# Kernel tuning notes

Measured on AMD Instinct MI355X. Metric: run time of the kernel, lower is better.

The kernel has to match this reference:

```python
import jax, jax.numpy as jnp
import numpy as np

N, T, DS, DA = 256, 64, 32, 8
D, H, FF = 512, 8, 2048
HD = D // H          # head_dim = 64
IN = DS + DA         # input_dim = 40
EULER_STEPS = 4


def setup_inputs():
    key = jax.random.key(0)
    ks = jax.random.split(key, 12)
    g = lambda k, shape: (jax.random.normal(k, shape) * 0.02).astype(jnp.float32)
    z = lambda *s: jnp.zeros(s, jnp.float32)
    o = lambda *s: jnp.ones(s, jnp.float32)
    return {
        "states": jax.random.normal(ks[0], (N, T, DS), jnp.float32),
        "actions": jax.random.normal(ks[1], (N, T, DA), jnp.float32),
        "time_steps": jnp.cumsum(jax.random.uniform(ks[2], (N, T + 1), jnp.float32, 0.01, 0.1), axis=1),
        "W_ode": g(ks[3], (D, D)), "b_ode": z(D),
        "W_in": g(ks[4], (IN, D)), "b_in": z(D),
        "ln_in_g": o(D), "ln_in_b": z(D),
        "W_q": g(ks[5], (D, D)), "b_q": z(D),
        "W_kv": g(ks[6], (IN + D, 2 * D + H)), "b_kv": z(2 * D + H),
        "W_out": g(ks[7], (D, D)), "b_out": z(D),
        "ln_ff_g": o(D), "ln_ff_b": z(D),
        "W_ff1": g(ks[8], (D, FF)), "b_ff1": z(FF),
        "W_ff2": g(ks[9], (FF, D)), "b_ff2": z(D),
        "W_dec": g(ks[10], (D, DS)), "b_dec": z(DS),
    }


def _ln(x, g, b):
    m = jnp.mean(x, -1, keepdims=True)
    v = jnp.mean((x - m) ** 2, -1, keepdims=True)
    return (x - m) * jax.lax.rsqrt(v + 1e-5) * g + b


def _forward(states, actions, time_steps, W_ode, b_ode, W_in, b_in, ln_in_g, ln_in_b,
             W_q, b_q, W_kv, b_kv, W_out, b_out, ln_ff_g, ln_ff_b,
             W_ff1, b_ff1, W_ff2, b_ff2, W_dec, b_dec):
    n = states.shape[0]
    # teacher forcing path (train=True, eps_decay=0): data_i = cat(states_i, actions_i)
    data_seq = jnp.concatenate([states, actions], -1).transpose(1, 0, 2)  # [T, N, IN]
    dts = (time_steps[:, 1:] - time_steps[:, :-1]).T                      # [T, N]

    def step(carry, xs):
        h1, W2 = carry            # h1: [N, D], W2: [N, H, HD, HD] fast weights
        data, dt = xs
        # integrate latent ODE over per-sample dt (fixed-step Euler, autonomous tanh MLP)
        step_dt = (dt / EULER_STEPS)[:, None]
        for _ in range(EULER_STEPS):
            h1 = h1 + step_dt * jnp.tanh(h1 @ W_ode + b_ode)
        # Hebbian fast-weight update: W2 += lr * v (x) k  (per head)
        x = jnp.concatenate([data, h1], -1)
        kvb = x @ W_kv + b_kv
        k = jax.nn.softmax(kvb[:, :D].reshape(n, H, HD), -1)
        v = jnp.tanh(kvb[:, D:2 * D]).reshape(n, H, HD)
        lr = jax.nn.sigmoid(kvb[:, 2 * D:])                    # [N, H]
        W2 = W2 + lr[:, :, None, None] * jnp.einsum('nhv,nhk->nhvk', v, k)
        # query_fast_weight
        q = _ln(data @ W_in + b_in, ln_in_g, ln_in_b) @ W_q + b_q
        q = jax.nn.softmax(q.reshape(n, H, HD), -1)
        out = jnp.einsum('nhvk,nhk->nhv', W2, q).reshape(n, D)
        out = out @ W_out + b_out
        y = _ln(out, ln_ff_g, ln_ff_b)
        out = jnp.maximum(y @ W_ff1 + b_ff1, 0.0) @ W_ff2 + b_ff2 + out  # FF block + residual
        pred = out @ W_dec + b_dec                              # decoder
        return (out, W2), pred

    h0 = jnp.zeros((n, D), states.dtype)
    W20 = jnp.zeros((n, H, HD, HD), states.dtype)
    _, preds = jax.lax.scan(step, (h0, W20), (data_seq, dts))
    return preds.transpose(1, 0, 2)  # [N, T, DS] predicted next states


def reference(states, actions, time_steps, W_ode, b_ode, W_in, b_in, ln_in_g, ln_in_b,
              W_q, b_q, W_kv, b_kv, W_out, b_out, ln_ff_g, ln_ff_b,
              W_ff1, b_ff1, W_ff2, b_ff2, W_dec, b_dec):
    return _forward(states, actions, time_steps, W_ode, b_ode, W_in, b_in, ln_in_g, ln_in_b,
                    W_q, b_q, W_kv, b_kv, W_out, b_out, ln_ff_g, ln_ff_b,
                    W_ff1, b_ff1, W_ff2, b_ff2, W_dec, b_dec)
```

## Files before the change

### kernel.cpp

```cpp
#include <hip/hip_runtime.h>

#define NS   256
#define TS   64
#define DS   32
#define DA   8
#define DD   512
#define HH   8
#define HD   64
#define FF   2048
#define INP  40
#define INPP 20
#define INPG 24
#define DP   256
#define KVKP 276
#define KVKPP 280
#define KVO  1032
#define FFP  1024

#define OFF_ODE 0
#define SZ_ODE  (32*512*8)
#define OFF_KV  (OFF_ODE+SZ_ODE)
#define SZ_KV   (35*1032*8)
#define OFF_IN  (OFF_KV+SZ_KV)
#define SZ_IN   (3*512*8)
#define OFF_Q   (OFF_IN+SZ_IN)
#define SZ_Q    (32*512*8)
#define OFF_OUT (OFF_Q+SZ_Q)
#define SZ_OUT  (32*512*8)
#define OFF_F1  (OFF_OUT+SZ_OUT)
#define SZ_F1   (32*2048*8)
#define OFF_F2  (OFF_F1+SZ_F1)
#define SZ_F2   (128*512*8)
#define OFF_DEC (OFF_F2+SZ_F2)
#define SZ_DEC  (32*32*8)

#define DEV __device__ __forceinline__

typedef _Float16 half2_t __attribute__((ext_vector_type(2)));

DEV half2_t as_h2(unsigned int u) { return __builtin_bit_cast(half2_t, u); }

DEV float dot2f(unsigned int w, unsigned int x, float acc) {
#if __has_builtin(__builtin_amdgcn_fdot2)
  return __builtin_amdgcn_fdot2(as_h2(w), as_h2(x), acc, false);
#else
  half2_t a = as_h2(w), b = as_h2(x);
  return acc + (float)a[0] * (float)b[0] + (float)a[1] * (float)b[1];
#endif
}

DEV unsigned int pack2f(float a, float b) {
  unsigned short ua = __builtin_bit_cast(unsigned short, (_Float16)a);
  unsigned short ub = __builtin_bit_cast(unsigned short, (_Float16)b);
  return ((unsigned int)ub << 16) | (unsigned int)ua;
}

DEV float fast_tanh(float x) {
  float ax = fabsf(x);
  float e  = __expf(-2.0f * ax);
  float r  = (1.0f - e) / (1.0f + e);
  return copysignf(r, x);
}

DEV float fast_sigmoid(float x) { return 1.0f / (1.0f + __expf(-x)); }

DEV float wave_max(float v) {
  #pragma unroll
  for (int o = 32; o; o >>= 1) v = fmaxf(v, __shfl_xor(v, o));
  return v;
}
DEV float wave_sum(float v) {
  #pragma unroll
  for (int o = 32; o; o >>= 1) v += __shfl_xor(v, o);
  return v;
}

DEV float dotG(const unsigned int* __restrict__ Wc, int strideG,
               const unsigned int* __restrict__ xq, int NG, float init) {
  float a0 = init, a1 = 0.f, a2 = 0.f, a3 = 0.f;
  #pragma unroll 4
  for (int g = 0; g < NG; ++g) {
    uint4 w0 = *reinterpret_cast<const uint4*>(Wc + g * strideG);
    uint4 w1 = *reinterpret_cast<const uint4*>(Wc + g * strideG + 4);
    uint4 x0 = *reinterpret_cast<const uint4*>(xq + g * 8);
    uint4 x1 = *reinterpret_cast<const uint4*>(xq + g * 8 + 4);
    a0 = dot2f(w0.x, x0.x, a0);
    a1 = dot2f(w0.y, x0.y, a1);
    a2 = dot2f(w0.z, x0.z, a2);
    a3 = dot2f(w0.w, x0.w, a3);
    a0 = dot2f(w1.x, x1.x, a0);
    a1 = dot2f(w1.y, x1.y, a1);
    a2 = dot2f(w1.z, x1.z, a2);
    a3 = dot2f(w1.w, x1.w, a3);
  }
  return (a0 + a1) + (a2 + a3);
}

__global__ void pack_wg_kernel(const float* __restrict__ src, unsigned int* __restrict__ dst,
                               int K, int KPpad, int Dout) {
  int idx = blockIdx.x * blockDim.x + threadIdx.x;
  int total = KPpad * Dout;
  if (idx >= total) return;
  int kp = idx / Dout;
  int j  = idx - kp * Dout;
  int r0 = 2 * kp, r1 = r0 + 1;
  float lo = (r0 < K) ? src[r0 * Dout + j] : 0.f;
  float hi = (r1 < K) ? src[r1 * Dout + j] : 0.f;
  int kg = kp >> 3, sub = kp & 7;
  dst[((kg * Dout + j) << 3) + sub] = pack2f(lo, hi);
}

__global__ __launch_bounds__(512) void fwp_main(
    const float* __restrict__ states, const float* __restrict__ actions,
    const float* __restrict__ tsteps,
    const float* __restrict__ b_ode, const float* __restrict__ b_in,
    const float* __restrict__ ln_in_g, const float* __restrict__ ln_in_b,
    const float* __restrict__ b_q, const float* __restrict__ b_kv,
    const float* __restrict__ b_out,
    const float* __restrict__ ln_ff_g, const float* __restrict__ ln_ff_b,
    const float* __restrict__ b_ff1, const float* __restrict__ b_ff2,
    const float* __restrict__ b_dec,
    const unsigned int* __restrict__ Wode, const unsigned int* __restrict__ Wkv,
    const unsigned int* __restrict__ Win,  const unsigned int* __restrict__ Wq,
    const unsigned int* __restrict__ Wout, const unsigned int* __restrict__ Wff1,
    const unsigned int* __restrict__ Wff2, const unsigned int* __restrict__ Wdec,
    unsigned int* __restrict__ ctrs, float* __restrict__ outp) {

  const int n = blockIdx.x, tid = threadIdx.x;
  const int w = tid >> 6, lane = tid & 63;

  __shared__ alignas(16) float        sh_h[DD];
  __shared__ alignas(16) unsigned int sh_hp[DP];
  __shared__ alignas(16) unsigned int sh_xp[KVKPP];
  __shared__ alignas(16) unsigned int sh_dp[INPG];
  __shared__ alignas(16) float        sh_t[DD];
  __shared__ alignas(16) unsigned int sh_p[DP];
  __shared__ alignas(16) float        sh_kvb[KVO];
  __shared__ alignas(16) float        sh_k[DD];
  __shared__ alignas(16) float        sh_v[DD];
  __shared__ alignas(16) float        sh_q[DD];
  __shared__ float                    sh_lr[HH];
  __shared__ alignas(16) float        sh_ff[FF];
  __shared__ alignas(16) unsigned int sh_ffp[FFP];
  __shared__ float                    sh_red[16];
  __shared__ alignas(16) float        sh_decp[512];
  __shared__ int                      sh_flag;

  float W2r[64];
  #pragma unroll
  for (int i = 0; i < 64; ++i) W2r[i] = 0.f;

  sh_h[tid] = 0.f;
  if (tid < DP) sh_hp[tid] = 0u;
  if (tid >= DP && tid < DP + (KVKPP - KVKP)) sh_xp[KVKP + (tid - DP)] = 0u;
  if (tid >= 300 && tid < 300 + (INPG - INPP)) sh_dp[INPP + (tid - 300)] = 0u;

  bool pace = true;
  unsigned int* ctr = ctrs + 16 * (n & 7);

  for (int t = 0; t < TS; ++t) {
    __syncthreads();

    if (pace) {
      if (tid == 0) {
        sh_flag = 0;
        __hip_atomic_fetch_add(ctr, 1u, __ATOMIC_RELAXED, __HIP_MEMORY_SCOPE_AGENT);
        unsigned int tgt = 32u * (unsigned int)(t + 1);
        int it = 0;
        while (__hip_atomic_load(ctr, __ATOMIC_RELAXED, __HIP_MEMORY_SCOPE_AGENT) < tgt) {
          if (++it > 4096) { sh_flag = 1; break; }
          __builtin_amdgcn_s_sleep(8);
        }
      }
      __syncthreads();
      if (sh_flag) pace = false;
    }

    if (tid < INPP) {
      int i0 = 2 * tid, i1 = i0 + 1;
      float a = (i0 < DS) ? states[(n * TS + t) * DS + i0] : actions[(n * TS + t) * DA + (i0 - DS)];
      float b = (i1 < DS) ? states[(n * TS + t) * DS + i1] : actions[(n * TS + t) * DA + (i1 - DS)];
      unsigned int p = pack2f(a, b);
      sh_xp[tid] = p;
      sh_dp[tid] = p;
    }
    const float sdt = 0.25f * (tsteps[n * (TS + 1) + t + 1] - tsteps[n * (TS + 1) + t]);

    for (int e = 0; e < 4; ++e) {
      float acc = dotG(Wode + tid * 8, DD * 8, sh_hp, 32, b_ode[tid]);
      sh_h[tid] += sdt * fast_tanh(acc);
      __syncthreads();
      if (tid < DP) sh_hp[tid] = pack2f(sh_h[2 * tid], sh_h[2 * tid + 1]);
      __syncthreads();
    }

    if (tid < DP) sh_xp[INPP + tid] = sh_hp[tid];
    __syncthreads();

    for (int j = tid; j < KVO; j += 512)
      sh_kvb[j] = dotG(Wkv + j * 8, KVO * 8, sh_xp, 35, b_kv[j]);
    __syncthreads();

    {
      float kx = sh_kvb[tid];
      float km = wave_max(kx);
      float ke = __expf(kx - km);
      float ks = wave_sum(ke);
      sh_k[tid] = ke / ks;
      sh_v[tid] = fast_tanh(sh_kvb[DD + tid]);
      if (tid < HH) sh_lr[tid] = fast_sigmoid(sh_kvb[2 * DD + tid]);
    }

    float y1 = dotG(Win + tid * 8, DD * 8, sh_dp, 3, b_in[tid]);
    {
      float s1 = y1, s2 = y1 * y1;
      #pragma unroll
      for (int o = 32; o; o >>= 1) { s1 += __shfl_xor(s1, o); s2 += __shfl_xor(s2, o); }
      if (lane == 0) { sh_red[2 * w] = s1; sh_red[2 * w + 1] = s2; }
      __syncthreads();
      s1 = 0.f; s2 = 0.f;
      #pragma unroll
      for (int i = 0; i < 8; ++i) { s1 += sh_red[2 * i]; s2 += sh_red[2 * i + 1]; }
      float m  = s1 * (1.0f / DD);
      float va = fmaxf(s2 * (1.0f / DD) - m * m, 0.f);
      float rs = rsqrtf(va + 1e-5f);
      sh_t[tid] = (y1 - m) * rs * ln_in_g[tid] + ln_in_b[tid];
    }
    __syncthreads();
    if (tid < DP) sh_p[tid] = pack2f(sh_t[2 * tid], sh_t[2 * tid + 1]);
    __syncthreads();
    {
      float qraw = dotG(Wq + tid * 8, DD * 8, sh_p, 32, b_q[tid]);
      float qm = wave_max(qraw);
      float qe = __expf(qraw - qm);
      float qs = wave_sum(qe);
      sh_q[tid] = qe / qs;
    }
    __syncthreads();

    {
      float vi  = sh_v[tid];
      float lrw = sh_lr[w];
      float lv  = lrw * vi;
      float acc = 0.f;
      const float* kb = sh_k + w * HD;
      const float* qb = sh_q + w * HD;
      #pragma unroll
      for (int jc = 0; jc < 16; ++jc) {
        float4 k4 = *reinterpret_cast<const float4*>(kb + 4 * jc);
        float4 q4 = *reinterpret_cast<const float4*>(qb + 4 * jc);
        W2r[4 * jc + 0] += lv * k4.x; acc += W2r[4 * jc + 0] * q4.x;
        W2r[4 * jc + 1] += lv * k4.y; acc += W2r[4 * jc + 1] * q4.y;
        W2r[4 * jc + 2] += lv * k4.z; acc += W2r[4 * jc + 2] * q4.z;
        W2r[4 * jc + 3] += lv * k4.w; acc += W2r[4 * jc + 3] * q4.w;
      }
      sh_t[tid] = acc;
    }
    __syncthreads();
    if (tid < DP) sh_p[tid] = pack2f(sh_t[2 * tid], sh_t[2 * tid + 1]);
    __syncthreads();

    float o1 = dotG(Wout + tid * 8, DD * 8, sh_p, 32, b_out[tid]);

    {
      float s1 = o1, s2 = o1 * o1;
      #pragma unroll
      for (int o = 32; o; o >>= 1) { s1 += __shfl_xor(s1, o); s2 += __shfl_xor(s2, o); }
      if (lane == 0) { sh_red[2 * w] = s1; sh_red[2 * w + 1] = s2; }
      __syncthreads();
      s1 = 0.f; s2 = 0.f;
      #pragma unroll
      for (int i = 0; i < 8; ++i) { s1 += sh_red[2 * i]; s2 += sh_red[2 * i + 1]; }
      float m  = s1 * (1.0f / DD);
      float va = fmaxf(s2 * (1.0f / DD) - m * m, 0.f);
      float rs = rsqrtf(va + 1e-5f);
      sh_t[tid] = (o1 - m) * rs * ln_ff_g[tid] + ln_ff_b[tid];
    }
    __syncthreads();
    if (tid < DP) sh_p[tid] = pack2f(sh_t[2 * tid], sh_t[2 * tid + 1]);
    __syncthreads();

    {
      float f0 = b_ff1[tid], f1 = b_ff1[tid + 512], f2 = b_ff1[tid + 1024], f3 = b_ff1[tid + 1536];
      #pragma unroll 2
      for (int g = 0; g < 32; ++g) {
        uint4 x0 = *reinterpret_cast<const uint4*>(sh_p + g * 8);
        uint4 x1 = *reinterpret_cast<const uint4*>(sh_p + g * 8 + 4);
        const unsigned int* wb = Wff1 + g * (FF * 8) + tid * 8;
        uint4 wa0 = *reinterpret_cast<const uint4*>(wb);
        uint4 wa1 = *reinterpret_cast<const uint4*>(wb + 4);
        uint4 wb0 = *reinterpret_cast<const uint4*>(wb + 512 * 8);
        uint4 wb1 = *reinterpret_cast<const uint4*>(wb + 512 * 8 + 4);
        uint4 wc0 = *reinterpret_cast<const uint4*>(wb + 1024 * 8);
        uint4 wc1 = *reinterpret_cast<const uint4*>(wb + 1024 * 8 + 4);
        uint4 wd0 = *reinterpret_cast<const uint4*>(wb + 1536 * 8);
        uint4 wd1 = *reinterpret_cast<const uint4*>(wb + 1536 * 8 + 4);
        f0 = dot2f(wa0.x, x0.x, f0); f0 = dot2f(wa0.y, x0.y, f0);
        f0 = dot2f(wa0.z, x0.z, f0); f0 = dot2f(wa0.w, x0.w, f0);
        f0 = dot2f(wa1.x, x1.x, f0); f0 = dot2f(wa1.y, x1.y, f0);
        f0 = dot2f(wa1.z, x1.z, f0); f0 = dot2f(wa1.w, x1.w, f0);
        f1 = dot2f(wb0.x, x0.x, f1); f1 = dot2f(wb0.y, x0.y, f1);
        f1 = dot2f(wb0.z, x0.z, f1); f1 = dot2f(wb0.w, x0.w, f1);
        f1 = dot2f(wb1.x, x1.x, f1); f1 = dot2f(wb1.y, x1.y, f1);
        f1 = dot2f(wb1.z, x1.z, f1); f1 = dot2f(wb1.w, x1.w, f1);
        f2 = dot2f(wc0.x, x0.x, f2); f2 = dot2f(wc0.y, x0.y, f2);
        f2 = dot2f(wc0.z, x0.z, f2); f2 = dot2f(wc0.w, x0.w, f2);
        f2 = dot2f(wc1.x, x1.x, f2); f2 = dot2f(wc1.y, x1.y, f2);
        f2 = dot2f(wc1.z, x1.z, f2); f2 = dot2f(wc1.w, x1.w, f2);
        f3 = dot2f(wd0.x, x0.x, f3); f3 = dot2f(wd0.y, x0.y, f3);
        f3 = dot2f(wd0.z, x0.z, f3); f3 = dot2f(wd0.w, x0.w, f3);
        f3 = dot2f(wd1.x, x1.x, f3); f3 = dot2f(wd1.y, x1.y, f3);
        f3 = dot2f(wd1.z, x1.z, f3); f3 = dot2f(wd1.w, x1.w, f3);
      }
      sh_ff[tid]        = fmaxf(f0, 0.f);
      sh_ff[tid + 512]  = fmaxf(f1, 0.f);
      sh_ff[tid + 1024] = fmaxf(f2, 0.f);
      sh_ff[tid + 1536] = fmaxf(f3, 0.f);
    }
    __syncthreads();
    sh_ffp[tid]       = pack2f(sh_ff[2 * tid], sh_ff[2 * tid + 1]);
    sh_ffp[tid + 512] = pack2f(sh_ff[2 * tid + 1024], sh_ff[2 * tid + 1025]);
    __syncthreads();

    {
      float o2 = dotG(Wff2 + tid * 8, DD * 8, sh_ffp, 128, b_ff2[tid]) + o1;
      sh_h[tid] = o2;
    }
    __syncthreads();
    if (tid < DP) sh_hp[tid] = pack2f(sh_h[2 * tid], sh_h[2 * tid + 1]);
    __syncthreads();

    {
      int col = tid & 31, ch = tid >> 5;
      const unsigned int* wbse = Wdec + col * 8;
      float a = 0.f;
      #pragma unroll
      for (int g = 2 * ch; g < 2 * ch + 2; ++g) {
        uint4 w0 = *reinterpret_cast<const uint4*>(wbse + g * (DS * 8));
        uint4 w1 = *reinterpret_cast<const uint4*>(wbse + g * (DS * 8) + 4);
        uint4 x0 = *reinterpret_cast<const uint4*>(sh_hp + g * 8);
        uint4 x1 = *reinterpret_cast<const uint4*>(sh_hp + g * 8 + 4);
        a = dot2f(w0.x, x0.x, a); a = dot2f(w0.y, x0.y, a);
        a = dot2f(w0.z, x0.z, a); a = dot2f(w0.w, x0.w, a);
        a = dot2f(w1.x, x1.x, a); a = dot2f(w1.y, x1.y, a);
        a = dot2f(w1.z, x1.z, a); a = dot2f(w1.w, x1.w, a);
      }
      sh_decp[tid] = a;
    }
    __syncthreads();
    if (tid < DS) {
      float s = b_dec[tid];
      #pragma unroll
      for (int c = 0; c < 16; ++c) s += sh_decp[c * 32 + tid];
      outp[(n * TS + t) * DS + tid] = s;
    }
  }
}

extern "C" void kernel_launch(void* const* d_in, const int* in_sizes, int n_in,
                              void* d_out, int out_size, void* d_ws, size_t ws_size,
                              hipStream_t stream) {
  (void)in_sizes; (void)n_in; (void)out_size; (void)ws_size;

  const float* states   = (const float*)d_in[0];
  const float* actions  = (const float*)d_in[1];
  const float* tsteps   = (const float*)d_in[2];
  const float* W_ode    = (const float*)d_in[3];
  const float* b_ode    = (const float*)d_in[4];
  const float* W_in     = (const float*)d_in[5];
  const float* b_in     = (const float*)d_in[6];
  const float* ln_in_g  = (const float*)d_in[7];
  const float* ln_in_b  = (const float*)d_in[8];
  const float* W_q      = (const float*)d_in[9];
  const float* b_q      = (const float*)d_in[10];
  const float* W_kv     = (const float*)d_in[11];
  const float* b_kv     = (const float*)d_in[12];
  const float* W_out    = (const float*)d_in[13];
  const float* b_out    = (const float*)d_in[14];
  const float* ln_ff_g  = (const float*)d_in[15];
  const float* ln_ff_b  = (const float*)d_in[16];
  const float* W_ff1    = (const float*)d_in[17];
  const float* b_ff1    = (const float*)d_in[18];
  const float* W_ff2    = (const float*)d_in[19];
  const float* b_ff2    = (const float*)d_in[20];
  const float* W_dec    = (const float*)d_in[21];
  const float* b_dec    = (const float*)d_in[22];

  unsigned int* wsbase = (unsigned int*)d_ws;
  unsigned int* ctrs   = wsbase;
  unsigned int* W      = wsbase + 128;

  hipMemsetAsync(d_ws, 0, 512, stream);

  auto launch_pack = [&](const float* src, unsigned int* dst, int K, int KPpad, int Dout) {
    int total = KPpad * Dout;
    int blocks = (total + 255) / 256;
    pack_wg_kernel<<<blocks, 256, 0, stream>>>(src, dst, K, KPpad, Dout);
  };

  launch_pack(W_ode, W + OFF_ODE, 512,  256, 512);
  launch_pack(W_kv,  W + OFF_KV,  552,  280, 1032);
  launch_pack(W_in,  W + OFF_IN,  40,   24,  512);
  launch_pack(W_q,   W + OFF_Q,   512,  256, 512);
  launch_pack(W_out, W + OFF_OUT, 512,  256, 512);
  launch_pack(W_ff1, W + OFF_F1,  512,  256, 2048);
  launch_pack(W_ff2, W + OFF_F2,  2048, 1024, 512);
  launch_pack(W_dec, W + OFF_DEC, 512,  256, 32);

  fwp_main<<<NS, 512, 0, stream>>>(
      states, actions, tsteps,
      b_ode, b_in, ln_in_g, ln_in_b, b_q, b_kv, b_out, ln_ff_g, ln_ff_b,
      b_ff1, b_ff2, b_dec,
      W + OFF_ODE, W + OFF_KV, W + OFF_IN, W + OFF_Q,
      W + OFF_OUT, W + OFF_F1, W + OFF_F2, W + OFF_DEC,
      ctrs, (float*)d_out);
}
```

Measured before the change: 5.905 ms.

## Double block size to 1024 threads with split-K partial sums per matvec

Launches 1024 threads per sample instead of 512. Each 512-output matvec (ODE, Wq, Wout, Wff2) is split along K between two thread halves, which combine their partial sums through shared memory. The per-thread Hebbian fast-weight row shrinks from 64 to 32 registers, and FF1 work is spread over twice as many threads. The goal is more latency hiding on weight streaming, at the cost of extra barriers and shared-memory reductions. Some reductions (layer-norm, softmax) still run on only half the threads.

Result: slower. 6.665 ms (+12.9%).

```diff
diff --git a/kernel.cpp b/kernel.cpp
--- a/kernel.cpp
+++ b/kernel.cpp
@@ -64,34 +64,21 @@
 
 DEV float fast_sigmoid(float x) { return 1.0f / (1.0f + __expf(-x)); }
 
-DEV float wave_max(float v) {
-  #pragma unroll
-  for (int o = 32; o; o >>= 1) v = fmaxf(v, __shfl_xor(v, o));
-  return v;
-}
-DEV float wave_sum(float v) {
-  #pragma unroll
-  for (int o = 32; o; o >>= 1) v += __shfl_xor(v, o);
-  return v;
-}
+#define LD4(p) (*reinterpret_cast<const uint4*>(p))
 
 DEV float dotG(const unsigned int* __restrict__ Wc, int strideG,
                const unsigned int* __restrict__ xq, int NG, float init) {
   float a0 = init, a1 = 0.f, a2 = 0.f, a3 = 0.f;
   #pragma unroll 4
   for (int g = 0; g < NG; ++g) {
-    uint4 w0 = *reinterpret_cast<const uint4*>(Wc + g * strideG);
-    uint4 w1 = *reinterpret_cast<const uint4*>(Wc + g * strideG + 4);
-    uint4 x0 = *reinterpret_cast<const uint4*>(xq + g * 8);
-    uint4 x1 = *reinterpret_cast<const uint4*>(xq + g * 8 + 4);
-    a0 = dot2f(w0.x, x0.x, a0);
-    a1 = dot2f(w0.y, x0.y, a1);
-    a2 = dot2f(w0.z, x0.z, a2);
-    a3 = dot2f(w0.w, x0.w, a3);
-    a0 = dot2f(w1.x, x1.x, a0);
-    a1 = dot2f(w1.y, x1.y, a1);
-    a2 = dot2f(w1.z, x1.z, a2);
-    a3 = dot2f(w1.w, x1.w, a3);
+    uint4 w0 = LD4(Wc + g * strideG);
+    uint4 w1 = LD4(Wc + g * strideG + 4);
+    uint4 x0 = LD4(xq + g * 8);
+    uint4 x1 = LD4(xq + g * 8 + 4);
+    a0 = dot2f(w0.x, x0.x, a0); a1 = dot2f(w0.y, x0.y, a1);
+    a2 = dot2f(w0.z, x0.z, a2); a3 = dot2f(w0.w, x0.w, a3);
+    a0 = dot2f(w1.x, x1.x, a0); a1 = dot2f(w1.y, x1.y, a1);
+    a2 = dot2f(w1.z, x1.z, a2); a3 = dot2f(w1.w, x1.w, a3);
   }
   return (a0 + a1) + (a2 + a3);
 }
@@ -110,7 +97,7 @@
   dst[((kg * Dout + j) << 3) + sub] = pack2f(lo, hi);
 }
 
-__global__ __launch_bounds__(512) void fwp_main(
+__global__ __launch_bounds__(1024, 4) void fwp_main(
     const float* __restrict__ states, const float* __restrict__ actions,
     const float* __restrict__ tsteps,
     const float* __restrict__ b_ode, const float* __restrict__ b_in,
@@ -128,6 +115,9 @@
 
   const int n = blockIdx.x, tid = threadIdx.x;
   const int w = tid >> 6, lane = tid & 63;
+  const int col = tid & 511;
+  const int sub = tid >> 9;
+  const int strideG = DD * 8;
 
   __shared__ alignas(16) float        sh_h[DD];
   __shared__ alignas(16) unsigned int sh_hp[DP];
@@ -143,17 +133,18 @@
   __shared__ alignas(16) float        sh_ff[FF];
   __shared__ alignas(16) unsigned int sh_ffp[FFP];
   __shared__ float                    sh_red[16];
-  __shared__ alignas(16) float        sh_decp[512];
+  __shared__ alignas(16) float        sh_decp[1024];
+  __shared__ alignas(16) float        sh_part[512];
   __shared__ int                      sh_flag;
 
-  float W2r[64];
+  float W2r[32];
   #pragma unroll
-  for (int i = 0; i < 64; ++i) W2r[i] = 0.f;
-
-  sh_h[tid] = 0.f;
+  for (int i = 0; i < 32; ++i) W2r[i] = 0.f;
+
+  if (tid < DD) sh_h[tid] = 0.f;
   if (tid < DP) sh_hp[tid] = 0u;
-  if (tid >= DP && tid < DP + (KVKPP - KVKP)) sh_xp[KVKP + (tid - DP)] = 0u;
-  if (tid >= 300 && tid < 300 + (INPG - INPP)) sh_dp[INPP + (tid - 300)] = 0u;
+  if (tid < (KVKPP - KVKP)) sh_xp[KVKP + tid] = 0u;
+  if (tid < (INPG - INPP))  sh_dp[INPP + tid] = 0u;
 
   bool pace = true;
   unsigned int* ctr = ctrs + 16 * (n & 7);
@@ -179,16 +170,19 @@
     if (tid < INPP) {
       int i0 = 2 * tid, i1 = i0 + 1;
       float a = (i0 < DS) ? states[(n * TS + t) * DS + i0] : actions[(n * TS + t) * DA + (i0 - DS)];
-      float b = (i1 < DS) ? states[(n * TS + t) * DS + i1] : actions[(n * TS + t) * DA + (i1 - DS)];
-      unsigned int p = pack2f(a, b);
+      float c = (i1 < DS) ? states[(n * TS + t) * DS + i1] : actions[(n * TS + t) * DA + (i1 - DS)];
+      unsigned int p = pack2f(a, c);
       sh_xp[tid] = p;
       sh_dp[tid] = p;
     }
     const float sdt = 0.25f * (tsteps[n * (TS + 1) + t + 1] - tsteps[n * (TS + 1) + t]);
 
     for (int e = 0; e < 4; ++e) {
-      float acc = dotG(Wode + tid * 8, DD * 8, sh_hp, 32, b_ode[tid]);
-      sh_h[tid] += sdt * fast_tanh(acc);
+      float acc = dotG(Wode + col * 8 + sub * 16 * strideG, strideG,
+                       sh_hp + sub * 128, 16, sub ? 0.f : b_ode[col]);
+      if (sub) sh_part[col] = acc;
+      __syncthreads();
+      if (!sub) sh_h[tid] += sdt * fast_tanh(acc + sh_part[tid]);
       __syncthreads();
       if (tid < DP) sh_hp[tid] = pack2f(sh_h[2 * tid], sh_h[2 * tid + 1]);
       __syncthreads();
@@ -197,56 +191,72 @@
     if (tid < DP) sh_xp[INPP + tid] = sh_hp[tid];
     __syncthreads();
 
-    for (int j = tid; j < KVO; j += 512)
+    for (int j = tid; j < KVO; j += 1024)
       sh_kvb[j] = dotG(Wkv + j * 8, KVO * 8, sh_xp, 35, b_kv[j]);
     __syncthreads();
 
-    {
+    if (tid < DD) {
       float kx = sh_kvb[tid];
-      float km = wave_max(kx);
+      float km = kx;
+      #pragma unroll
+      for (int o = 32; o; o >>= 1) km = fmaxf(km, __shfl_xor(km, o));
       float ke = __expf(kx - km);
-      float ks = wave_sum(ke);
+      float ks = ke;
+      #pragma unroll
+      for (int o = 32; o; o >>= 1) ks += __shfl_xor(ks, o);
       sh_k[tid] = ke / ks;
       sh_v[tid] = fast_tanh(sh_kvb[DD + tid]);
-      if (tid < HH) sh_lr[tid] = fast_sigmoid(sh_kvb[2 * DD + tid]);
-    }
-
-    float y1 = dotG(Win + tid * 8, DD * 8, sh_dp, 3, b_in[tid]);
-    {
+    }
+    if (tid < HH) sh_lr[tid] = fast_sigmoid(sh_kvb[2 * DD + tid]);
+
+    {
+      float y1 = 0.f;
+      if (tid < DD) y1 = dotG(Win + tid * 8, strideG, sh_dp, 3, b_in[tid]);
       float s1 = y1, s2 = y1 * y1;
       #pragma unroll
       for (int o = 32; o; o >>= 1) { s1 += __shfl_xor(s1, o); s2 += __shfl_xor(s2, o); }
-      if (lane == 0) { sh_red[2 * w] = s1; sh_red[2 * w + 1] = s2; }
-      __syncthreads();
-      s1 = 0.f; s2 = 0.f;
-      #pragma unroll
-      for (int i = 0; i < 8; ++i) { s1 += sh_red[2 * i]; s2 += sh_red[2 * i + 1]; }
-      float m  = s1 * (1.0f / DD);
-      float va = fmaxf(s2 * (1.0f / DD) - m * m, 0.f);
-      float rs = rsqrtf(va + 1e-5f);
-      sh_t[tid] = (y1 - m) * rs * ln_in_g[tid] + ln_in_b[tid];
+      if (tid < DD && lane == 0) { sh_red[2 * w] = s1; sh_red[2 * w + 1] = s2; }
+      __syncthreads();
+      if (tid < DD) {
+        float t1 = 0.f, t2 = 0.f;
+        #pragma unroll
+        for (int i = 0; i < 8; ++i) { t1 += sh_red[2 * i]; t2 += sh_red[2 * i + 1]; }
+        float m  = t1 * (1.0f / DD);
+        float va = fmaxf(t2 * (1.0f / DD) - m * m, 0.f);
+        float rs = rsqrtf(va + 1e-5f);
+        sh_t[tid] = (y1 - m) * rs * ln_in_g[tid] + ln_in_b[tid];
+      }
     }
     __syncthreads();
     if (tid < DP) sh_p[tid] = pack2f(sh_t[2 * tid], sh_t[2 * tid + 1]);
     __syncthreads();
     {
-      float qraw = dotG(Wq + tid * 8, DD * 8, sh_p, 32, b_q[tid]);
-      float qm = wave_max(qraw);
-      float qe = __expf(qraw - qm);
-      float qs = wave_sum(qe);
-      sh_q[tid] = qe / qs;
-    }
-    __syncthreads();
-
-    {
-      float vi  = sh_v[tid];
-      float lrw = sh_lr[w];
-      float lv  = lrw * vi;
+      float qacc = dotG(Wq + col * 8 + sub * 16 * strideG, strideG,
+                        sh_p + sub * 128, 16, sub ? 0.f : b_q[col]);
+      if (sub) sh_part[col] = qacc;
+      __syncthreads();
+      if (!sub) {
+        float qt = qacc + sh_part[tid];
+        float qm = qt;
+        #pragma unroll
+        for (int o = 32; o; o >>= 1) qm = fmaxf(qm, __shfl_xor(qm, o));
+        float qe = __expf(qt - qm);
+        float qs = qe;
+        #pragma unroll
+        for (int o = 32; o; o >>= 1) qs += __shfl_xor(qs, o);
+        sh_q[tid] = qe / qs;
+      }
+    }
+    __syncthreads();
+
+    {
+      int hh = w >> 1, kh = (w & 1) << 5;
+      float lv = sh_lr[hh] * sh_v[(hh << 6) + lane];
       float acc = 0.f;
-      const float* kb = sh_k + w * HD;
-      const float* qb = sh_q + w * HD;
-      #pragma unroll
-      for (int jc = 0; jc < 16; ++jc) {
+      const float* kb = sh_k + (hh << 6) + kh;
+      const float* qb = sh_q + (hh << 6) + kh;
+      #pragma unroll
+      for (int jc = 0; jc < 8; ++jc) {
         float4 k4 = *reinterpret_cast<const float4*>(kb + 4 * jc);
         float4 q4 = *reinterpret_cast<const float4*>(qb + 4 * jc);
         W2r[4 * jc + 0] += lv * k4.x; acc += W2r[4 * jc + 0] * q4.x;
@@ -254,104 +264,100 @@
         W2r[4 * jc + 2] += lv * k4.z; acc += W2r[4 * jc + 2] * q4.z;
         W2r[4 * jc + 3] += lv * k4.w; acc += W2r[4 * jc + 3] * q4.w;
       }
-      sh_t[tid] = acc;
+      if (!(w & 1)) sh_part[(hh << 6) + lane] = acc;
+      __syncthreads();
+      if (w & 1) sh_t[(hh << 6) + lane] = acc + sh_part[(hh << 6) + lane];
     }
     __syncthreads();
     if (tid < DP) sh_p[tid] = pack2f(sh_t[2 * tid], sh_t[2 * tid + 1]);
     __syncthreads();
 
-    float o1 = dotG(Wout + tid * 8, DD * 8, sh_p, 32, b_out[tid]);
+    float o1 = 0.f;
+    {
+      float oacc = dotG(Wout + col * 8 + sub * 16 * strideG, strideG,
+                        sh_p + sub * 128, 16, sub ? 0.f : b_out[col]);
+      if (sub) sh_part[col] = oacc;
+      __syncthreads();
+      if (!sub) o1 = oacc + sh_part[tid];
+    }
 
     {
       float s1 = o1, s2 = o1 * o1;
       #pragma unroll
       for (int o = 32; o; o >>= 1) { s1 += __shfl_xor(s1, o); s2 += __shfl_xor(s2, o); }
-      if (lane == 0) { sh_red[2 * w] = s1; sh_red[2 * w + 1] = s2; }
-      __syncthreads();
-      s1 = 0.f; s2 = 0.f;
-      #pragma unroll
-      for (int i = 0; i < 8; ++i) { s1 += sh_red[2 * i]; s2 += sh_red[2 * i + 1]; }
-      float m  = s1 * (1.0f / DD);
-      float va = fmaxf(s2 * (1.0f / DD) - m * m, 0.f);
-      float rs = rsqrtf(va + 1e-5f);
-      sh_t[tid] = (o1 - m) * rs * ln_ff_g[tid] + ln_ff_b[tid];
+      if (tid < DD && lane == 0) { sh_red[2 * w] = s1; sh_red[2 * w + 1] = s2; }
+      __syncthreads();
+      if (tid < DD) {
+        float t1 = 0.f, t2 = 0.f;
+        #pragma unroll
+        for (int i = 0; i < 8; ++i) { t1 += sh_red[2 * i]; t2 += sh_red[2 * i + 1]; }
+        float m  = t1 * (1.0f / DD);
+        float va = fmaxf(t2 * (1.0f / DD) - m * m, 0.f);
+        float rs = rsqrtf(va + 1e-5f);
+        sh_t[tid] = (o1 - m) * rs * ln_ff_g[tid] + ln_ff_b[tid];
+      }
     }
     __syncthreads();
     if (tid < DP) sh_p[tid] = pack2f(sh_t[2 * tid], sh_t[2 * tid + 1]);
     __syncthreads();
 
     {
-      float f0 = b_ff1[tid], f1 = b_ff1[tid + 512], f2 = b_ff1[tid + 1024], f3 = b_ff1[tid + 1536];
+      float f0 = b_ff1[tid], f1 = b_ff1[tid + 1024];
       #pragma unroll 2
       for (int g = 0; g < 32; ++g) {
-        uint4 x0 = *reinterpret_cast<const uint4*>(sh_p + g * 8);
-        uint4 x1 = *reinterpret_cast<const uint4*>(sh_p + g * 8 + 4);
         const unsigned int* wb = Wff1 + g * (FF * 8) + tid * 8;
-        uint4 wa0 = *reinterpret_cast<const uint4*>(wb);
-        uint4 wa1 = *reinterpret_cast<const uint4*>(wb + 4);
-        uint4 wb0 = *reinterpret_cast<const uint4*>(wb + 512 * 8);
-        uint4 wb1 = *reinterpret_cast<const uint4*>(wb + 512 * 8 + 4);
-        uint4 wc0 = *reinterpret_cast<const uint4*>(wb + 1024 * 8);
-        uint4 wc1 = *reinterpret_cast<const uint4*>(wb + 1024 * 8 + 4);
-        uint4 wd0 = *reinterpret_cast<const uint4*>(wb + 1536 * 8);
-        uint4 wd1 = *reinterpret_cast<const uint4*>(wb + 1536 * 8 + 4);
-        f0 = dot2f(wa0.x, x0.x, f0); f0 = dot2f(wa0.y, x0.y, f0);
-        f0 = dot2f(wa0.z, x0.z, f0); f0 = dot2f(wa0.w, x0.w, f0);
-        f0 = dot2f(wa1.x, x1.x, f0); f0 = dot2f(wa1.y, x1.y, f0);
-        f0 = dot2f(wa1.z, x1.z, f0); f0 = dot2f(wa1.w, x1.w, f0);
-        f1 = dot2f(wb0.x, x0.x, f1); f1 = dot2f(wb0.y, x0.y, f1);
-        f1 = dot2f(wb0.z, x0.z, f1); f1 = dot2f(wb0.w, x0.w, f1);
-        f1 = dot2f(wb1.x, x1.x, f1); f1 = dot2f(wb1.y, x1.y, f1);
-        f1 = dot2f(wb1.z, x1.z, f1); f1 = dot2f(wb1.w, x1.w, f1);
-        f2 = dot2f(wc0.x, x0.x, f2); f2 = dot2f(wc0.y, x0.y, f2);
-        f2 = dot2f(wc0.z, x0.z, f2); f2 = dot2f(wc0.w, x0.w, f2);
-        f2 = dot2f(wc1.x, x1.x, f2); f2 = dot2f(wc1.y, x1.y, f2);
-        f2 = dot2f(wc1.z, x1.z, f2); f2 = dot2f(wc1.w, x1.w, f2);
-        f3 = dot2f(wd0.x, x0.x, f3); f3 = dot2f(wd0.y, x0.y, f3);
-        f3 = dot2f(wd0.z, x0.z, f3); f3 = dot2f(wd0.w, x0.w, f3);
-        f3 = dot2f(wd1.x, x1.x, f3); f3 = dot2f(wd1.y, x1.y, f3);
-        f3 = dot2f(wd1.z, x1.z, f3); f3 = dot2f(wd1.w, x1.w, f3);
+        uint4 w00 = LD4(wb);
+        uint4 w01 = LD4(wb + 4);
+        uint4 w10 = LD4(wb + 1024 * 8);
+        uint4 w11 = LD4(wb + 1024 * 8 + 4);
+        uint4 x0 = LD4(sh_p + g * 8);
+        uint4 x1 = LD4(sh_p + g * 8 + 4);
+        f0 = dot2f(w00.x, x0.x, f0); f0 = dot2f(w00.y, x0.y, f0);
+        f0 = dot2f(w00.z, x0.z, f0); f0 = dot2f(w00.w, x0.w, f0);
+        f0 = dot2f(w01.x, x1.x, f0); f0 = dot2f(w01.y, x1.y, f0);
+        f0 = dot2f(w01.z, x1.z, f0); f0 = dot2f(w01.w, x1.w, f0);
+        f1 = dot2f(w10.x, x0.x, f1); f1 = dot2f(w10.y, x0.y, f1);
+        f1 = dot2f(w10.z, x0.z, f1); f1 = dot2f(w10.w, x0.w, f1);
+        f1 = dot2f(w11.x, x1.x, f1); f1 = dot2f(w11.y, x1.y, f1);
+        f1 = dot2f(w11.z, x1.z, f1); f1 = dot2f(w11.w, x1.w, f1);
       }
       sh_ff[tid]        = fmaxf(f0, 0.f);
-      sh_ff[tid + 512]  = fmaxf(f1, 0.f);
-      sh_ff[tid + 1024] = fmaxf(f2, 0.f);
-      sh_ff[tid + 1536] = fmaxf(f3, 0.f);
-    }
-    __syncthreads();
-    sh_ffp[tid]       = pack2f(sh_ff[2 * tid], sh_ff[2 * tid + 1]);
-    sh_ffp[tid + 512] = pack2f(sh_ff[2 * tid + 1024], sh_ff[2 * tid + 1025]);
-    __syncthreads();
-
-    {
-      float o2 = dotG(Wff2 + tid * 8, DD * 8, sh_ffp, 128, b_ff2[tid]) + o1;
-      sh_h[tid] = o2;
+      sh_ff[tid + 1024] = fmaxf(f1, 0.f);
+    }
+    __syncthreads();
+    sh_ffp[tid] = pack2f(sh_ff[2 * tid], sh_ff[2 * tid + 1]);
+    __syncthreads();
+
+    {
+      float oacc = dotG(Wff2 + col * 8 + sub * 64 * strideG, strideG,
+                        sh_ffp + sub * 512, 64, sub ? 0.f : b_ff2[col]);
+      if (sub) sh_part[col] = oacc;
+      __syncthreads();
+      if (!sub) sh_h[tid] = oacc + sh_part[tid] + o1;
     }
     __syncthreads();
     if (tid < DP) sh_hp[tid] = pack2f(sh_h[2 * tid], sh_h[2 * tid + 1]);
     __syncthreads();
 
     {
-      int col = tid & 31, ch = tid >> 5;
-      const unsigned int* wbse = Wdec + col * 8;
+      int colD = tid & 31, ch = tid >> 5;
+      const unsigned int* wb = Wdec + colD * 8 + ch * (DS * 8);
+      uint4 w0 = LD4(wb);
+      uint4 w1 = LD4(wb + 4);
+      uint4 x0 = LD4(sh_hp + ch * 8);
+      uint4 x1 = LD4(sh_hp + ch * 8 + 4);
       float a = 0.f;
-      #pragma unroll
-      for (int g = 2 * ch; g < 2 * ch + 2; ++g) {
-        uint4 w0 = *reinterpret_cast<const uint4*>(wbse + g * (DS * 8));
-        uint4 w1 = *reinterpret_cast<const uint4*>(wbse + g * (DS * 8) + 4);
-        uint4 x0 = *reinterpret_cast<const uint4*>(sh_hp + g * 8);
-        uint4 x1 = *reinterpret_cast<const uint4*>(sh_hp + g * 8 + 4);
-        a = dot2f(w0.x, x0.x, a); a = dot2f(w0.y, x0.y, a);
-        a = dot2f(w0.z, x0.z, a); a = dot2f(w0.w, x0.w, a);
-        a = dot2f(w1.x, x1.x, a); a = dot2f(w1.y, x1.y, a);
-        a = dot2f(w1.z, x1.z, a); a = dot2f(w1.w, x1.w, a);
-      }
+      a = dot2f(w0.x, x0.x, a); a = dot2f(w0.y, x0.y, a);
+      a = dot2f(w0.z, x0.z, a); a = dot2f(w0.w, x0.w, a);
+      a = dot2f(w1.x, x1.x, a); a = dot2f(w1.y, x1.y, a);
+      a = dot2f(w1.z, x1.z, a); a = dot2f(w1.w, x1.w, a);
       sh_decp[tid] = a;
     }
     __syncthreads();
     if (tid < DS) {
       float s = b_dec[tid];
       #pragma unroll
-      for (int c = 0; c < 16; ++c) s += sh_decp[c * 32 + tid];
+      for (int c = 0; c < 32; ++c) s += sh_decp[c * 32 + tid];
       outp[(n * TS + t) * DS + tid] = s;
     }
   }
@@ -407,7 +413,7 @@
   launch_pack(W_ff2, W + OFF_F2,  2048, 1024, 512);
   launch_pack(W_dec, W + OFF_DEC, 512,  256, 32);
 
-  fwp_main<<<NS, 512, 0, stream>>>(
+  fwp_main<<<NS, 1024, 0, stream>>>(
       states, actions, tsteps,
       b_ode, b_in, ln_in_g, ln_in_b, b_q, b_kv, b_out, ln_ff_g, ln_ff_b,
       b_ff1, b_ff2, b_dec,
```
